# Kernel tuning notes

Hardware: AMD Instinct MI355X
Metric: run time of the kernel (lower is better)

Reference implementation:

```python
import jax, jax.numpy as jnp
import numpy as np

N_NODES = 100000
N_EDGES = 1600000
IN_DIM = 29
OUT_DIM = 64
BN_EPS = 1e-5


def setup_inputs() -> dict:
    key = jax.random.key(0)
    k1, k2, k3, k4, k5, k6, k7, k8 = jax.random.split(key, 8)
    node = jax.random.normal(k1, (N_NODES, 3), dtype=jnp.float32)
    features = jax.random.normal(k2, (N_NODES, IN_DIM), dtype=jnp.float32)
    edges = jax.random.randint(k3, (N_EDGES, 2), 0, N_NODES, dtype=jnp.int64)
    # Linear(input_dim+3, output_dim, bias=False): weight [out, in+3]
    fan_in = IN_DIM + 3
    weight = jax.random.uniform(k4, (OUT_DIM, fan_in), dtype=jnp.float32,
                                minval=-1.0, maxval=1.0) / np.sqrt(fan_in)
    # BatchNorm1d(output_dim) in eval mode: affine params + running stats
    gamma = jax.random.normal(k5, (OUT_DIM,), dtype=jnp.float32) * 0.1 + 1.0
    beta = jax.random.normal(k6, (OUT_DIM,), dtype=jnp.float32) * 0.1
    running_mean = jax.random.normal(k7, (OUT_DIM,), dtype=jnp.float32) * 0.1
    running_var = jax.random.uniform(k8, (OUT_DIM,), dtype=jnp.float32,
                                     minval=0.5, maxval=1.5)
    return {"node": node, "features": features, "edges": edges,
            "weight": weight, "gamma": gamma, "beta": beta,
            "running_mean": running_mean, "running_var": running_var}


def reference(node, features, edges, weight, gamma, beta, running_mean, running_var):
    dst = edges[:, 0]  # pos_i index (pooling destination)
    src = edges[:, 1]  # pos_j / x_j index
    # gather + concat: msg [E, in+3]
    msg = jnp.concatenate([features[src], node[src] - node[dst]], axis=1)
    # Linear (no bias): [E, out]
    msg = jnp.einsum('ei,oi->eo', msg, weight)
    # BatchNorm1d (eval mode, running stats)
    inv_std = gamma / jnp.sqrt(running_var + BN_EPS)
    msg = (msg - running_mean) * inv_std + beta
    # scatter-max pooling over destination nodes (fixed N segments;
    # torch.unique + scatter_reduce(amax) == segment_max restricted to covered
    # nodes; empty segments filled with 0 matching the zeros init)
    pooled = jax.ops.segment_max(msg, dst, num_segments=N_NODES)
    return jnp.where(jnp.isneginf(pooled), 0.0, pooled)
```

## Files before the change

### kernel.cpp

```cpp
#include <hip/hip_runtime.h>
#include <hip/hip_fp16.h>

#define IN_DIM 29
#define XDIM 32
#define OUT_DIM 64
#define BN_EPS 1e-5f

#define BW      32
#define BW_LOG  5
#define TBLK    2048
#define MAXBUCK 4096
#define SENT    0


__global__ __launch_bounds__(256) void fused_tc_kernel(
    const float* __restrict__ features, const float* __restrict__ node,
    const float* __restrict__ weight, const float* __restrict__ gamma,
    const float* __restrict__ rvar, unsigned short* __restrict__ yq,
    const int* __restrict__ edges, int* __restrict__ gHist,
    int n_nodes, int npw, int n_edges, int nbuck, int chunk, int nblk)
{
    if ((int)blockIdx.x < nblk) {
        __shared__ int h[MAXBUCK];
        for (int i = threadIdx.x; i < nbuck; i += 256) h[i] = 0;
        __syncthreads();
        const int e0 = blockIdx.x * chunk;
        const int e1 = min(e0 + chunk, n_edges);
        for (int e = e0 + threadIdx.x; e < e1; e += 256)
            atomicAdd(&h[edges[2*e] >> BW_LOG], 1);
        __syncthreads();
        for (int i = threadIdx.x; i < nbuck; i += 256)
            gHist[i * nblk + blockIdx.x] = h[i];
    } else {
        const int lane = threadIdx.x & 63;
        const int wave = (((int)blockIdx.x - nblk) * 256 + (int)threadIdx.x) >> 6;
        int n0 = wave * npw;
        int n1 = n0 + npw; if (n1 > n_nodes) n1 = n_nodes;

        float w[XDIM];
        const float4* wp = (const float4*)(weight + lane * XDIM);
#pragma unroll
        for (int q = 0; q < 8; ++q) {
            float4 v = wp[q];
            w[4*q+0] = v.x; w[4*q+1] = v.y; w[4*q+2] = v.z; w[4*q+3] = v.w;
        }
        const float a = gamma[lane] * __frsqrt_rn(rvar[lane] + BN_EPS);

        for (int n = n0; n < n1; ++n) {
            const float* f = features + (size_t)n * IN_DIM;
            float acc = 0.0f;
#pragma unroll
            for (int i = 0; i < IN_DIM; ++i) acc = fmaf(f[i], w[i], acc);
            const float* nd = node + (size_t)n * 3;
#pragma unroll
            for (int j = 0; j < 3; ++j) acc = fmaf(nd[j], w[IN_DIM + j], acc);
            unsigned short hh = __half_as_ushort(__float2half(acc * a));
            unsigned short enc = (hh & 0x8000) ? (unsigned short)(~hh)
                                               : (unsigned short)(hh | 0x8000);
            yq[(size_t)n * OUT_DIM + lane] = enc;
        }
    }
}

__global__ __launch_bounds__(256) void scan_a_kernel(
    int* __restrict__ data, int n, int* __restrict__ aux)
{
    const int t = threadIdx.x;
    const int base = blockIdx.x * 1024 + t * 4;
    int v[4];
#pragma unroll
    for (int k = 0; k < 4; ++k) v[k] = (base + k < n) ? data[base + k] : 0;
    int tsum = v[0] + v[1] + v[2] + v[3];

    const int lane = t & 63, wv = t >> 6;
    int x = tsum;
#pragma unroll
    for (int off = 1; off < 64; off <<= 1) {
        int y = __shfl_up(x, off);
        if (lane >= off) x += y;
    }
    __shared__ int wsum[4];
    if (lane == 63) wsum[wv] = x;
    __syncthreads();
    int wexcl = 0;
    for (int i = 0; i < wv; ++i) wexcl += wsum[i];
    int run = wexcl + x - tsum;
#pragma unroll
    for (int k = 0; k < 4; ++k) {
        if (base + k < n) data[base + k] = run;
        run += v[k];
    }
    if (t == 255) aux[blockIdx.x] = run;
}

__global__ __launch_bounds__(256) void scan_b_kernel(int* __restrict__ aux, int nb) {
    const int t = threadIdx.x;
    const int lane = t & 63, wv = t >> 6;
    __shared__ int wsum[4];
    __shared__ int s_run;
    if (t == 0) s_run = 0;
    __syncthreads();
    for (int base = 0; base < nb; base += 256) {
        const int i = base + t;
        int v = (i < nb) ? aux[i] : 0;
        int x = v;
#pragma unroll
        for (int off = 1; off < 64; off <<= 1) {
            int y = __shfl_up(x, off);
            if (lane >= off) x += y;
        }
        if (lane == 63) wsum[wv] = x;
        __syncthreads();
        int wexcl = 0;
        for (int k = 0; k < wv; ++k) wexcl += wsum[k];
        const int run = s_run;
        if (i < nb) aux[i] = run + wexcl + x - v;
        __syncthreads();
        if (t == 255) s_run = run + wexcl + x;
        __syncthreads();
    }
}

__global__ __launch_bounds__(512) void partition_kernel(
    const int* __restrict__ edges, const int* __restrict__ gOffs,
    const int* __restrict__ aux,
    int* __restrict__ keys, int n_edges, int nbuck, int chunk, int nblk)
{
    __shared__ int cur[MAXBUCK];
    for (int i = threadIdx.x; i < nbuck; i += 512) {
        const int idx = i * nblk + blockIdx.x;
        cur[i] = gOffs[idx] + aux[idx >> 10];
    }
    __syncthreads();
    const int e0 = blockIdx.x * chunk;
    const int e1 = min(e0 + chunk, n_edges);
    for (int e = e0 + threadIdx.x; e < e1; e += 512) {
        const int dst = edges[2*e], src = edges[2*e+1];
        const int b = dst >> BW_LOG;
        const int pos = atomicAdd(&cur[b], 1);
        keys[pos] = (dst & (BW - 1)) | (src << BW_LOG);
    }
}

__global__ __launch_bounds__(256) void pool_fused_kernel(
    const int* __restrict__ gOffs, const int* __restrict__ aux,
    const int* __restrict__ keys,
    const unsigned short* __restrict__ yq, const float* __restrict__ node,
    const float* __restrict__ weight, const float* __restrict__ gamma,
    const float* __restrict__ beta, const float* __restrict__ rmean,
    const float* __restrict__ rvar,
    float* __restrict__ out, int n_nodes, int n_edges, int nbuck, int nblk)
{
    __shared__ int acc[BW * OUT_DIM];
    const int tid = threadIdx.x;
    const int lane = tid & 63, wid = tid >> 6;
    const int b = blockIdx.x;

    {
        int4* p = (int4*)acc;
        for (int i = tid; i < BW * OUT_DIM / 4; i += 256)
            p[i] = make_int4(SENT, SENT, SENT, SENT);
    }
    __syncthreads();

    const int i0 = b * nblk;
    const int beg = gOffs[i0] + aux[i0 >> 10];
    int end;
    if (b == nbuck - 1) end = n_edges;
    else {
        const int i1 = (b + 1) * nblk;
        end = gOffs[i1] + aux[i1 >> 10];
    }

    const int cnt = end - beg;
    const int slice = (cnt + 3) >> 2;
    const int w_beg = beg + wid * slice;
    const int w_end = min(w_beg + slice, end);

    if (w_beg < w_end) {
        const int last = w_end - 1;
        int j = w_beg;
        int kv = keys[min(j + lane, last)];
        while (j < w_end) {
            const int jn = j + 64;
            int kv_n = 0;
            if (jn < w_end) kv_n = keys[min(jn + lane, last)];
            const int m = w_end - j < 64 ? w_end - j : 64;
            const int ng = (m + 7) >> 3;

            unsigned int va[8]; int da[8];
#pragma unroll
            for (int u = 0; u < 8; ++u) {
                const int uu = (u < m) ? u : (m - 1);
                const int key = __builtin_amdgcn_readlane(kv, uu);
                da[u] = key & (BW - 1);
                va[u] = yq[(size_t)((unsigned)key >> BW_LOG) * OUT_DIM + lane];
            }
            for (int g = 0; g < ng; ++g) {
                unsigned int vb[8]; int db[8];
                const bool more = (g + 1 < ng);
                if (more) {
#pragma unroll
                    for (int u = 0; u < 8; ++u) {
                        int uu = (g + 1) * 8 + u; uu = (uu < m) ? uu : (m - 1);
                        const int key = __builtin_amdgcn_readlane(kv, uu);
                        db[u] = key & (BW - 1);
                        vb[u] = yq[(size_t)((unsigned)key >> BW_LOG) * OUT_DIM + lane];
                    }
                }
#pragma unroll
                for (int u = 0; u < 8; ++u)
                    atomicMax(&acc[da[u] * OUT_DIM + lane], (int)va[u]);
                if (more) {
#pragma unroll
                    for (int u = 0; u < 8; ++u) { va[u] = vb[u]; da[u] = db[u]; }
                }
            }
            j = jn; kv = kv_n;
        }
    }
    __syncthreads();

    const float a  = gamma[lane] * __frsqrt_rn(rvar[lane] + BN_EPS);
    const float bp = beta[lane] - rmean[lane] * a;
    const float w29 = weight[lane * XDIM + 29] * a;
    const float w30 = weight[lane * XDIM + 30] * a;
    const float w31 = weight[lane * XDIM + 31] * a;

    for (int d = wid; d < BW; d += 4) {
        const int dg = b * BW + d;
        if (dg >= n_nodes) break;
        const int k = acc[d * OUT_DIM + lane];
        float rr;
        if (k == SENT) {
            rr = 0.0f;
        } else {
            const unsigned short enc = (unsigned short)k;
            const unsigned short h = (enc & 0x8000) ? (unsigned short)(enc ^ 0x8000)
                                                    : (unsigned short)(~enc);
            const float v = __half2float(__ushort_as_half(h));
            const float nx = node[(size_t)dg * 3 + 0];
            const float ny = node[(size_t)dg * 3 + 1];
            const float nz = node[(size_t)dg * 3 + 2];
            rr = v + (bp - (w29 * nx + w30 * ny + w31 * nz));
        }
        out[(size_t)dg * OUT_DIM + lane] = rr;
    }
}

__global__ void init_kernel(int4* __restrict__ out, int total4) {
    int t = blockIdx.x * blockDim.x + threadIdx.x;
    if (t < total4) out[t] = make_int4(INT_MIN, INT_MIN, INT_MIN, INT_MIN);
}

__global__ __launch_bounds__(256) void edge_atomic_kernel(
    const int* __restrict__ edges,
    const float* __restrict__ features, const float* __restrict__ node,
    const float* __restrict__ weight, const float* __restrict__ gamma,
    const float* __restrict__ beta, const float* __restrict__ rmean,
    const float* __restrict__ rvar,
    int* __restrict__ out, int n_edges, int epw)
{
    const int lane = threadIdx.x & 63;
    const int wave = (blockIdx.x * blockDim.x + threadIdx.x) >> 6;
    int e0 = wave * epw, e1 = e0 + epw;
    if (e1 > n_edges) e1 = n_edges;

    float w[XDIM];
    const float4* wp = (const float4*)(weight + lane * XDIM);
#pragma unroll
    for (int q = 0; q < 8; ++q) {
        float4 v = wp[q];
        w[4*q+0] = v.x; w[4*q+1] = v.y; w[4*q+2] = v.z; w[4*q+3] = v.w;
    }
    const float a = gamma[lane] * __frsqrt_rn(rvar[lane] + BN_EPS);
    const float bprime = beta[lane] - rmean[lane] * a;

    for (int e = e0; e < e1; ++e) {
        const int dst = edges[2*e+0], src = edges[2*e+1];
        float x[XDIM];
#pragma unroll
        for (int i = 0; i < IN_DIM; ++i) x[i] = features[(size_t)src * IN_DIM + i];
#pragma unroll
        for (int j = 0; j < 3; ++j)
            x[IN_DIM+j] = node[(size_t)src*3+j] - node[(size_t)dst*3+j];
        float acc = 0.0f;
#pragma unroll
        for (int i = 0; i < XDIM; ++i) acc = fmaf(x[i], w[i], acc);
        float msg = fmaf(acc, a, bprime);
        int bb = __float_as_int(msg);
        int key = (bb < 0) ? (bb ^ 0x7FFFFFFF) : bb;
        atomicMax(out + (size_t)dst * OUT_DIM + lane, key);
    }
}

__global__ void decode_kernel(int* __restrict__ out, int total) {
    int t = blockIdx.x * blockDim.x + threadIdx.x;
    if (t >= total) return;
    int k = out[t];
    float r;
    if (k == INT_MIN) r = 0.0f;
    else { int b = (k < 0) ? (k ^ 0x7FFFFFFF) : k; r = __int_as_float(b); }
    ((float*)out)[t] = r;
}

extern "C" void kernel_launch(void* const* d_in, const int* in_sizes, int n_in,
                              void* d_out, int out_size, void* d_ws, size_t ws_size,
                              hipStream_t stream) {
    const float* node     = (const float*)d_in[0];
    const float* features = (const float*)d_in[1];
    const int*   edges    = (const int*)d_in[2];
    const float* weight   = (const float*)d_in[3];
    const float* gamma    = (const float*)d_in[4];
    const float* beta     = (const float*)d_in[5];
    const float* rmean    = (const float*)d_in[6];
    const float* rvar     = (const float*)d_in[7];

    const int n_nodes = in_sizes[0] / 3;
    const int n_edges = in_sizes[2] / 2;

    const int nbuck = (n_nodes + BW - 1) >> BW_LOG;

    int nblk = 0; size_t o_yq=0, o_hist=0, o_aux=0, o_keys=0; size_t need = 0;
    for (int cand = 128; cand >= 32; cand >>= 1) {
        const int n_scan = nbuck * cand;
        const int nb_scan = (n_scan + 1023) / 1024;
        size_t off = 0;
        auto alloc = [&](size_t bytes) { size_t r = off; off = (off + bytes + 15) & ~(size_t)15; return r; };
        o_yq   = alloc((size_t)n_nodes * OUT_DIM * sizeof(unsigned short));
        o_hist = alloc((size_t)n_scan * sizeof(int));
        o_aux  = alloc((size_t)nb_scan * sizeof(int));
        o_keys = alloc((size_t)n_edges * sizeof(int));
        need = off;
        if (need <= ws_size) { nblk = cand; break; }
    }

    if (nblk > 0 && nbuck <= MAXBUCK && n_nodes <= MAXBUCK * BW) {
        const int n_scan = nbuck * nblk;
        const int nb_scan = (n_scan + 1023) / 1024;
        const int chunk = (n_edges + nblk - 1) / nblk;
        const int npw = (n_nodes + TBLK * 4 - 1) / (TBLK * 4);

        char* base  = (char*)d_ws;
        unsigned short* yq = (unsigned short*)(base + o_yq);
        int* gHist  = (int*)(base + o_hist);
        int* aux    = (int*)(base + o_aux);
        int* keys   = (int*)(base + o_keys);

        fused_tc_kernel<<<nblk + TBLK, 256, 0, stream>>>(
            features, node, weight, gamma, rvar, yq,
            edges, gHist, n_nodes, npw, n_edges, nbuck, chunk, nblk);
        scan_a_kernel<<<nb_scan, 256, 0, stream>>>(gHist, n_scan, aux);
        scan_b_kernel<<<1, 256, 0, stream>>>(aux, nb_scan);
        partition_kernel<<<nblk, 512, 0, stream>>>(edges, gHist, aux, keys,
                                                   n_edges, nbuck, chunk, nblk);
        pool_fused_kernel<<<nbuck, 256, 0, stream>>>(
            gHist, aux, keys, yq, node, weight, gamma, beta, rmean, rvar,
            (float*)d_out, n_nodes, n_edges, nbuck, nblk);
    } else {
        int* out_i = (int*)d_out;
        const int total4 = out_size / 4;
        init_kernel<<<(total4 + 255) / 256, 256, 0, stream>>>((int4*)out_i, total4);
        const int n_waves = 8192;
        const int epw = (n_edges + n_waves - 1) / n_waves;
        edge_atomic_kernel<<<n_waves / 4, 256, 0, stream>>>(
            edges, features, node, weight, gamma, beta, rmean, rvar,
            out_i, n_edges, epw);
        decode_kernel<<<(out_size + 255) / 256, 256, 0, stream>>>(out_i, out_size);
    }
}
```

Before: 193.3 us.

## Decouple histogram block count from partition block count with wider partition blocks

The edge-count histogram now runs over up to 512 chunks (cblk), giving more blocks in the fused histogram/transform kernel. The partition kernel still uses a fixed 128 blocks, now with 1024 threads each, and each block takes R consecutive histogram chunks. It reads its starting offsets from the first of its sub-chunks. The cost is a larger histogram and scan, since the scan size grows with cblk, and 64-bit index math.

Result: slower. 211.4 us (+9.4%).

```diff
diff --git a/kernel.cpp b/kernel.cpp
--- a/kernel.cpp
+++ b/kernel.cpp
@@ -8,6 +8,7 @@
 
 #define BW      32
 #define BW_LOG  5
+#define PBLK    128
 #define TBLK    2048
 #define MAXBUCK 4096
 #define SENT    0
@@ -18,22 +19,22 @@
     const float* __restrict__ weight, const float* __restrict__ gamma,
     const float* __restrict__ rvar, unsigned short* __restrict__ yq,
     const int* __restrict__ edges, int* __restrict__ gHist,
-    int n_nodes, int npw, int n_edges, int nbuck, int chunk, int nblk)
-{
-    if ((int)blockIdx.x < nblk) {
+    int n_nodes, int npw, int n_edges, int nbuck, int chunk_c, int cblk)
+{
+    if ((int)blockIdx.x < cblk) {
         __shared__ int h[MAXBUCK];
         for (int i = threadIdx.x; i < nbuck; i += 256) h[i] = 0;
         __syncthreads();
-        const int e0 = blockIdx.x * chunk;
-        const int e1 = min(e0 + chunk, n_edges);
+        const int e0 = blockIdx.x * chunk_c;
+        const int e1 = min(e0 + chunk_c, n_edges);
         for (int e = e0 + threadIdx.x; e < e1; e += 256)
             atomicAdd(&h[edges[2*e] >> BW_LOG], 1);
         __syncthreads();
         for (int i = threadIdx.x; i < nbuck; i += 256)
-            gHist[i * nblk + blockIdx.x] = h[i];
+            gHist[(size_t)i * cblk + blockIdx.x] = h[i];
     } else {
         const int lane = threadIdx.x & 63;
-        const int wave = (((int)blockIdx.x - nblk) * 256 + (int)threadIdx.x) >> 6;
+        const int wave = (((int)blockIdx.x - cblk) * 256 + (int)threadIdx.x) >> 6;
         int n0 = wave * npw;
         int n1 = n0 + npw; if (n1 > n_nodes) n1 = n_nodes;
 
@@ -121,20 +122,22 @@
     }
 }
 
-__global__ __launch_bounds__(512) void partition_kernel(
+__global__ __launch_bounds__(1024) void partition_kernel(
     const int* __restrict__ edges, const int* __restrict__ gOffs,
     const int* __restrict__ aux,
-    int* __restrict__ keys, int n_edges, int nbuck, int chunk, int nblk)
+    int* __restrict__ keys, int n_edges, int nbuck, int chunk_c, int cblk)
 {
     __shared__ int cur[MAXBUCK];
-    for (int i = threadIdx.x; i < nbuck; i += 512) {
-        const int idx = i * nblk + blockIdx.x;
+    const int R = cblk / PBLK;
+    for (int i = threadIdx.x; i < nbuck; i += 1024) {
+        const size_t idx = (size_t)i * cblk + R * blockIdx.x;
         cur[i] = gOffs[idx] + aux[idx >> 10];
     }
     __syncthreads();
-    const int e0 = blockIdx.x * chunk;
-    const int e1 = min(e0 + chunk, n_edges);
-    for (int e = e0 + threadIdx.x; e < e1; e += 512) {
+    const int chunk_p = R * chunk_c;
+    const int e0 = blockIdx.x * chunk_p;
+    const int e1 = min(e0 + chunk_p, n_edges);
+    for (int e = e0 + threadIdx.x; e < e1; e += 1024) {
         const int dst = edges[2*e], src = edges[2*e+1];
         const int b = dst >> BW_LOG;
         const int pos = atomicAdd(&cur[b], 1);
@@ -149,7 +152,7 @@
     const float* __restrict__ weight, const float* __restrict__ gamma,
     const float* __restrict__ beta, const float* __restrict__ rmean,
     const float* __restrict__ rvar,
-    float* __restrict__ out, int n_nodes, int n_edges, int nbuck, int nblk)
+    float* __restrict__ out, int n_nodes, int n_edges, int nbuck, int cblk)
 {
     __shared__ int acc[BW * OUT_DIM];
     const int tid = threadIdx.x;
@@ -163,12 +166,12 @@
     }
     __syncthreads();
 
-    const int i0 = b * nblk;
+    const size_t i0 = (size_t)b * cblk;
     const int beg = gOffs[i0] + aux[i0 >> 10];
     int end;
     if (b == nbuck - 1) end = n_edges;
     else {
-        const int i1 = (b + 1) * nblk;
+        const size_t i1 = (size_t)(b + 1) * cblk;
         end = gOffs[i1] + aux[i1 >> 10];
     }
 
@@ -321,24 +324,23 @@
 
     const int nbuck = (n_nodes + BW - 1) >> BW_LOG;
 
-    int nblk = 0; size_t o_yq=0, o_hist=0, o_aux=0, o_keys=0; size_t need = 0;
-    for (int cand = 128; cand >= 32; cand >>= 1) {
-        const int n_scan = nbuck * cand;
-        const int nb_scan = (n_scan + 1023) / 1024;
+    int cblk = 0; size_t o_yq=0, o_hist=0, o_aux=0, o_keys=0;
+    for (int cand = 512; cand >= PBLK; cand >>= 1) {
+        const size_t n_scan = (size_t)nbuck * cand;
+        const size_t nb_scan = (n_scan + 1023) / 1024;
         size_t off = 0;
         auto alloc = [&](size_t bytes) { size_t r = off; off = (off + bytes + 15) & ~(size_t)15; return r; };
         o_yq   = alloc((size_t)n_nodes * OUT_DIM * sizeof(unsigned short));
-        o_hist = alloc((size_t)n_scan * sizeof(int));
-        o_aux  = alloc((size_t)nb_scan * sizeof(int));
+        o_hist = alloc(n_scan * sizeof(int));
+        o_aux  = alloc(nb_scan * sizeof(int));
         o_keys = alloc((size_t)n_edges * sizeof(int));
-        need = off;
-        if (need <= ws_size) { nblk = cand; break; }
-    }
-
-    if (nblk > 0 && nbuck <= MAXBUCK && n_nodes <= MAXBUCK * BW) {
-        const int n_scan = nbuck * nblk;
+        if (off <= ws_size) { cblk = cand; break; }
+    }
+
+    if (cblk > 0 && nbuck <= MAXBUCK && n_nodes <= MAXBUCK * BW) {
+        const int n_scan = nbuck * cblk;
         const int nb_scan = (n_scan + 1023) / 1024;
-        const int chunk = (n_edges + nblk - 1) / nblk;
+        const int chunk_c = (n_edges + cblk - 1) / cblk;
         const int npw = (n_nodes + TBLK * 4 - 1) / (TBLK * 4);
 
         char* base  = (char*)d_ws;
@@ -347,16 +349,16 @@
         int* aux    = (int*)(base + o_aux);
         int* keys   = (int*)(base + o_keys);
 
-        fused_tc_kernel<<<nblk + TBLK, 256, 0, stream>>>(
+        fused_tc_kernel<<<cblk + TBLK, 256, 0, stream>>>(
             features, node, weight, gamma, rvar, yq,
-            edges, gHist, n_nodes, npw, n_edges, nbuck, chunk, nblk);
+            edges, gHist, n_nodes, npw, n_edges, nbuck, chunk_c, cblk);
         scan_a_kernel<<<nb_scan, 256, 0, stream>>>(gHist, n_scan, aux);
         scan_b_kernel<<<1, 256, 0, stream>>>(aux, nb_scan);
-        partition_kernel<<<nblk, 512, 0, stream>>>(edges, gHist, aux, keys,
-                                                   n_edges, nbuck, chunk, nblk);
+        partition_kernel<<<PBLK, 1024, 0, stream>>>(edges, gHist, aux, keys,
+                                                    n_edges, nbuck, chunk_c, cblk);
         pool_fused_kernel<<<nbuck, 256, 0, stream>>>(
             gHist, aux, keys, yq, node, weight, gamma, beta, rmean, rvar,
-            (float*)d_out, n_nodes, n_edges, nbuck, nblk);
+            (float*)d_out, n_nodes, n_edges, nbuck, cblk);
     } else {
         int* out_i = (int*)d_out;
         const int total4 = out_size / 4;
```
